# Performance work log

Hardware: AMD Instinct MI355X
Metric: run time of the kernel (lower is better)

The kernel has to match this reference:

```python
import jax, jax.numpy as jnp
import numpy as np

B, N, IN_DIM, EMB, HEADS, M, ITERS = 8, 4096, 1024, 512, 4, 256, 6
DH = EMB // HEADS
SCALE = DH ** -0.5
RES_K = 33  # residual depthwise conv kernel size (TransMIL / nystrom-attention default)


def setup_inputs() -> dict:
    key = jax.random.key(0)
    ks = iter(jax.random.split(key, 40))
    def rn(shape, s=0.02):
        return jax.random.normal(next(ks), shape, jnp.float32) * s
    inp = {"X": jax.random.normal(next(ks), (B, N, IN_DIM), jnp.float32)}
    inp["few_w"] = rn((IN_DIM, EMB)); inp["few_b"] = jnp.zeros((EMB,), jnp.float32)
    inp["cls_token"] = rn((1, 1, EMB), 1.0)
    for i in (1, 2):
        inp[f"l{i}_ln_g"] = jnp.ones((EMB,), jnp.float32)
        inp[f"l{i}_ln_b"] = jnp.zeros((EMB,), jnp.float32)
        inp[f"l{i}_qkv_w"] = rn((EMB, 3 * EMB))
        inp[f"l{i}_out_w"] = rn((EMB, EMB))
        inp[f"l{i}_out_b"] = jnp.zeros((EMB,), jnp.float32)
        inp[f"l{i}_res_k"] = rn((HEADS, 1, RES_K, 1))
    for ksz in (7, 5, 3):
        inp[f"ppeg_k{ksz}"] = rn((EMB, 1, ksz, ksz))
        inp[f"ppeg_b{ksz}"] = jnp.zeros((EMB,), jnp.float32)
    inp["norm_g"] = jnp.ones((EMB,), jnp.float32)
    inp["norm_b"] = jnp.zeros((EMB,), jnp.float32)
    inp["cls_w"] = rn((EMB, 1)); inp["cls_b"] = jnp.zeros((1,), jnp.float32)
    return inp


def _ln(x, g, b):
    mu = x.mean(-1, keepdims=True)
    var = x.var(-1, keepdims=True)
    return (x - mu) / jnp.sqrt(var + 1e-5) * g + b


def _pinv(x, iters):
    # Moore-Penrose iterative pseudo-inverse of (..., m, m)
    abs_x = jnp.abs(x)
    z = jnp.swapaxes(x, -1, -2) / (abs_x.sum(-1).max() * abs_x.sum(-2).max())
    I = jnp.eye(x.shape[-1], dtype=x.dtype)
    for _ in range(iters):
        xz = x @ z
        z = 0.25 * z @ (13 * I - xz @ (15 * I - xz @ (7 * I - xz)))
    return z


def _nystrom_layer(x, ln_g, ln_b, qkv_w, out_w, out_b, res_k):
    # pre-norm transformer layer with Nystrom attention + residual depthwise conv
    b, n, d = x.shape
    h = _ln(x, ln_g, ln_b)
    pad = (-n) % M  # left-pad so seq divisible by n_landmarks
    hp = jnp.pad(h, ((0, 0), (pad, 0), (0, 0)))
    n_p = n + pad
    q, k, v = jnp.split(hp @ qkv_w, 3, axis=-1)
    def to_heads(t):
        return t.reshape(b, n_p, HEADS, DH).transpose(0, 2, 1, 3)  # (b,h,n,dh)
    q, k, v = to_heads(q) * SCALE, to_heads(k), to_heads(v)
    l = n_p // M
    q_l = q.reshape(b, HEADS, M, l, DH).mean(3)  # landmark means
    k_l = k.reshape(b, HEADS, M, l, DH).mean(3)
    a1 = jax.nn.softmax(jnp.einsum('bhid,bhjd->bhij', q, k_l), -1)    # (b,h,n,m)
    a2 = jax.nn.softmax(jnp.einsum('bhid,bhjd->bhij', q_l, k_l), -1)  # (b,h,m,m)
    a3 = jax.nn.softmax(jnp.einsum('bhid,bhjd->bhij', q_l, k), -1)    # (b,h,m,n)
    out = a1 @ (_pinv(a2, ITERS) @ (a3 @ v))
    # residual depthwise conv over sequence, one channel per head
    res = jax.lax.conv_general_dilated(
        v, res_k, (1, 1), ((RES_K // 2, RES_K // 2), (0, 0)),
        dimension_numbers=('NCHW', 'OIHW', 'NCHW'), feature_group_count=HEADS)
    out = out + res
    out = out.transpose(0, 2, 1, 3).reshape(b, n_p, d) @ out_w + out_b
    return x + out[:, -n:]


def _dwconv(x, k, bias, pad):
    y = jax.lax.conv_general_dilated(
        x, k, (1, 1), ((pad, pad), (pad, pad)),
        dimension_numbers=('NCHW', 'OIHW', 'NCHW'), feature_group_count=EMB)
    return y + bias[None, :, None, None]


def _ppeg(x, H, W, k7, b7, k5, b5, k3, b3):
    b, _, c = x.shape
    cls_t, feat = x[:, :1], x[:, 1:]
    f = feat.transpose(0, 2, 1).reshape(b, c, H, W)
    y = f + _dwconv(f, k7, b7, 3) + _dwconv(f, k5, b5, 2) + _dwconv(f, k3, b3, 1)
    y = y.reshape(b, c, H * W).transpose(0, 2, 1)
    return jnp.concatenate([cls_t, y], axis=1)


def _forward(X, few_w, few_b, cls_token,
             l1_ln_g, l1_ln_b, l1_qkv_w, l1_out_w, l1_out_b, l1_res_k,
             l2_ln_g, l2_ln_b, l2_qkv_w, l2_out_w, l2_out_b, l2_res_k,
             ppeg_k7, ppeg_b7, ppeg_k5, ppeg_b5, ppeg_k3, ppeg_b3,
             norm_g, norm_b, cls_w, cls_b):
    b, bag = X.shape[0], X.shape[1]
    h = X @ few_w + few_b
    ps = int(np.ceil(np.sqrt(bag)))
    add = ps * ps - bag
    h = jnp.concatenate([h, h[:, :add]], axis=1)  # pad bag to perfect square
    h = jnp.concatenate([jnp.broadcast_to(cls_token, (b, 1, EMB)), h], axis=1)
    h = _nystrom_layer(h, l1_ln_g, l1_ln_b, l1_qkv_w, l1_out_w, l1_out_b, l1_res_k)
    h = _ppeg(h, ps, ps, ppeg_k7, ppeg_b7, ppeg_k5, ppeg_b5, ppeg_k3, ppeg_b3)
    h = _nystrom_layer(h, l2_ln_g, l2_ln_b, l2_qkv_w, l2_out_w, l2_out_b, l2_res_k)
    h = _ln(h, norm_g, norm_b)
    return (h[:, 0] @ cls_w + cls_b).squeeze(-1)  # (batch,) bag logits


def reference(X, few_w, few_b, cls_token,
              l1_ln_g, l1_ln_b, l1_qkv_w, l1_out_w, l1_out_b, l1_res_k,
              l2_ln_g, l2_ln_b, l2_qkv_w, l2_out_w, l2_out_b, l2_res_k,
              ppeg_k7, ppeg_b7, ppeg_k5, ppeg_b5, ppeg_k3, ppeg_b3,
              norm_g, norm_b, cls_w, cls_b):
    return _forward(X, few_w, few_b, cls_token,
                    l1_ln_g, l1_ln_b, l1_qkv_w, l1_out_w, l1_out_b, l1_res_k,
                    l2_ln_g, l2_ln_b, l2_qkv_w, l2_out_w, l2_out_b, l2_res_k,
                    ppeg_k7, ppeg_b7, ppeg_k5, ppeg_b5, ppeg_k3, ppeg_b3,
                    norm_g, norm_b, cls_w, cls_b)
```

## Files before the change

kernel.cpp:

```cpp
#include <hip/hip_runtime.h>

constexpr int BATCH = 8;
constexpr int NTOK  = 4097;
constexpr int NP    = 4352;
constexpr int PADR  = 255;
constexpr int EMBD  = 512;
constexpr int DHD   = 128;
constexpr int LSUB  = 17;
constexpr float SCALE_F = 0.08838834764831845f;

constexpr int PPS   = 72;
constexpr int PPLN  = 72 * 70;
constexpr long long TPAD_FLOATS = (long long)BATCH * EMBD * PPLN;

typedef unsigned short u16;
typedef short   s16x8 __attribute__((ext_vector_type(8)));
typedef u16     u16x4 __attribute__((ext_vector_type(4)));
typedef float   f32x4 __attribute__((ext_vector_type(4)));

__device__ __forceinline__ u16 f2bf(float x) {
    unsigned u = __float_as_uint(x);
    u += 0x7fffu + ((u >> 16) & 1u);
    return (u16)(u >> 16);
}
__device__ __forceinline__ float bf2f(u16 h) {
    return __uint_as_float(((unsigned)h) << 16);
}

__device__ __forceinline__ void gload16(const u16* gp, u16* lp) {
    __builtin_amdgcn_global_load_lds(
        (const __attribute__((address_space(1))) unsigned int*)gp,
        (__attribute__((address_space(3))) unsigned int*)lp,
        16, 0, 0);
}

__device__ __forceinline__ float block_sum256(float v) {
    __shared__ float tmp[4];
    __syncthreads();
#pragma unroll
    for (int off = 32; off > 0; off >>= 1) v += __shfl_down(v, off, 64);
    int t = threadIdx.x;
    if ((t & 63) == 0) tmp[t >> 6] = v;
    __syncthreads();
    return tmp[0] + tmp[1] + tmp[2] + tmp[3];
}

__device__ __forceinline__ float block_max256(float v) {
    __shared__ float tmp[4];
    __syncthreads();
#pragma unroll
    for (int off = 32; off > 0; off >>= 1) v = fmaxf(v, __shfl_down(v, off, 64));
    int t = threadIdx.x;
    if ((t & 63) == 0) tmp[t >> 6] = v;
    __syncthreads();
    return fmaxf(fmaxf(tmp[0], tmp[1]), fmaxf(tmp[2], tmp[3]));
}

struct GemmP {
    const float* A; const float* B; float* C; const float* bias;
    long long As1, As2, Bs1, Bs2, Cs1, Cs2;
    int Adiv, Bdiv, Cdiv;
    int Am, Bk, Bn, Cm, Arow, Crow;
    int M, N, K, nb;
    float alpha; int accum;
    float bdiagc; int btrans; float cdiagc; int ctrans;
};

constexpr int LDSTR = 40;
constexpr int AH = 0, AL = 2560, BHs = 5120, BLs = 7680;

__global__ __launch_bounds__(256) void gemm_k(GemmP p) {
    __shared__ u16 lds[10240];
    const int bz = blockIdx.z;
    const float* Ab = p.A + (long long)(bz / p.Adiv) * p.As1 + (long long)(bz % p.Adiv) * p.As2;
    const float* Bb = p.B + (long long)(bz / p.Bdiv) * p.Bs1 + (long long)(bz % p.Bdiv) * p.Bs2;
    float*       Cb = p.C + (long long)(bz / p.Cdiv) * p.Cs1 + (long long)(bz % p.Cdiv) * p.Cs2;
    const int m0 = blockIdx.y * 64, n0 = blockIdx.x * 64;
    const int t = threadIdx.x;
    const int wave = t >> 6, lane = t & 63;
    const int wm = (wave & 1) * 32, wn = (wave >> 1) * 32;
    const int quad = lane >> 4, l15 = lane & 15;

    f32x4 acc[2][2];
#pragma unroll
    for (int i = 0; i < 2; ++i)
#pragma unroll
        for (int j = 0; j < 2; ++j) acc[i][j] = (f32x4){0.f, 0.f, 0.f, 0.f};

    for (int k0 = 0; k0 < p.K; k0 += 32) {
        {
            const int ar = t >> 2, ac = (t & 3) * 8;
            float v[8];
            if (m0 + ar < p.M) {
                const float* s = Ab + (long long)(m0 + ar + p.Arow) * p.Am + (k0 + ac);
                float4 x0 = *(const float4*)s, x1 = *(const float4*)(s + 4);
                v[0] = x0.x; v[1] = x0.y; v[2] = x0.z; v[3] = x0.w;
                v[4] = x1.x; v[5] = x1.y; v[6] = x1.z; v[7] = x1.w;
            } else {
#pragma unroll
                for (int i = 0; i < 8; ++i) v[i] = 0.f;
            }
            u16 h[8], l[8];
#pragma unroll
            for (int i = 0; i < 8; ++i) { h[i] = f2bf(v[i]); l[i] = f2bf(v[i] - bf2f(h[i])); }
            const int off = ar * LDSTR + ac;
            u16x4 a0, a1, b0, b1;
#pragma unroll
            for (int i = 0; i < 4; ++i) { a0[i] = h[i]; a1[i] = h[i + 4]; b0[i] = l[i]; b1[i] = l[i + 4]; }
            *(u16x4*)&lds[AH + off] = a0; *(u16x4*)&lds[AH + off + 4] = a1;
            *(u16x4*)&lds[AL + off] = b0; *(u16x4*)&lds[AL + off + 4] = b1;
        }
        if (p.Bn == 1) {
            const int bk = t >> 3, n8 = (t & 7) * 8;
            const float* s = Bb + (long long)(k0 + bk) * p.Bk + (n0 + n8);
            float4 x0 = *(const float4*)s, x1 = *(const float4*)(s + 4);
            float v[8] = {x0.x, x0.y, x0.z, x0.w, x1.x, x1.y, x1.z, x1.w};
            if (p.btrans) {
                const int gk = k0 + bk;
#pragma unroll
                for (int i = 0; i < 8; ++i)
                    v[i] = (gk == n0 + n8 + i ? p.bdiagc : 0.f) - v[i];
            }
#pragma unroll
            for (int i = 0; i < 8; ++i) {
                int j = (i + (t & 7)) & 7;
                u16 h = f2bf(v[j]);
                lds[BHs + (n8 + j) * LDSTR + bk] = h;
                lds[BLs + (n8 + j) * LDSTR + bk] = f2bf(v[j] - bf2f(h));
            }
        } else {
            const int bn = t >> 2, k8 = (t & 3) * 8;
            const float* s = Bb + (long long)(n0 + bn) * p.Bn + (k0 + k8);
            float4 x0 = *(const float4*)s, x1 = *(const float4*)(s + 4);
            float v[8] = {x0.x, x0.y, x0.z, x0.w, x1.x, x1.y, x1.z, x1.w};
            u16 h[8], l[8];
#pragma unroll
            for (int i = 0; i < 8; ++i) { h[i] = f2bf(v[i]); l[i] = f2bf(v[i] - bf2f(h[i])); }
            const int off = bn * LDSTR + k8;
            u16x4 a0, a1, b0, b1;
#pragma unroll
            for (int i = 0; i < 4; ++i) { a0[i] = h[i]; a1[i] = h[i + 4]; b0[i] = l[i]; b1[i] = l[i + 4]; }
            *(u16x4*)&lds[BHs + off] = a0; *(u16x4*)&lds[BHs + off + 4] = a1;
            *(u16x4*)&lds[BLs + off] = b0; *(u16x4*)&lds[BLs + off + 4] = b1;
        }
        __syncthreads();

        s16x8 ah[2], al[2], bh[2], bl[2];
#pragma unroll
        for (int mi = 0; mi < 2; ++mi) {
            const int off = (wm + mi * 16 + l15) * LDSTR + quad * 8;
            u16x4 q0 = *(const u16x4*)&lds[AH + off], q1 = *(const u16x4*)&lds[AH + off + 4];
            u16x4 r0 = *(const u16x4*)&lds[AL + off], r1 = *(const u16x4*)&lds[AL + off + 4];
            s16x8 fh, fl;
#pragma unroll
            for (int i = 0; i < 4; ++i) { fh[i] = q0[i]; fh[i + 4] = q1[i]; fl[i] = r0[i]; fl[i + 4] = r1[i]; }
            ah[mi] = fh; al[mi] = fl;
        }
#pragma unroll
        for (int ni = 0; ni < 2; ++ni) {
            const int off = (wn + ni * 16 + l15) * LDSTR + quad * 8;
            u16x4 q0 = *(const u16x4*)&lds[BHs + off], q1 = *(const u16x4*)&lds[BHs + off + 4];
            u16x4 r0 = *(const u16x4*)&lds[BLs + off], r1 = *(const u16x4*)&lds[BLs + off + 4];
            s16x8 fh, fl;
#pragma unroll
            for (int i = 0; i < 4; ++i) { fh[i] = q0[i]; fh[i + 4] = q1[i]; fl[i] = r0[i]; fl[i + 4] = r1[i]; }
            bh[ni] = fh; bl[ni] = fl;
        }
#pragma unroll
        for (int mi = 0; mi < 2; ++mi)
#pragma unroll
            for (int ni = 0; ni < 2; ++ni) {
                acc[mi][ni] = __builtin_amdgcn_mfma_f32_16x16x32_bf16(ah[mi], bh[ni], acc[mi][ni], 0, 0, 0);
                acc[mi][ni] = __builtin_amdgcn_mfma_f32_16x16x32_bf16(ah[mi], bl[ni], acc[mi][ni], 0, 0, 0);
                acc[mi][ni] = __builtin_amdgcn_mfma_f32_16x16x32_bf16(al[mi], bh[ni], acc[mi][ni], 0, 0, 0);
            }
        __syncthreads();
    }

#pragma unroll
    for (int mi = 0; mi < 2; ++mi)
#pragma unroll
        for (int ni = 0; ni < 2; ++ni) {
            const int n = n0 + wn + ni * 16 + l15;
#pragma unroll
            for (int r = 0; r < 4; ++r) {
                const int m = m0 + wm + mi * 16 + quad * 4 + r;
                if (m >= p.M) continue;
                float v = p.alpha * acc[mi][ni][r];
                if (p.bias) v += p.bias[n];
                if (p.ctrans) v = (m == n ? p.cdiagc : 0.f) - v;
                float* dst = Cb + (long long)(m + p.Crow) * p.Cm + n;
                if (p.accum) *dst += v; else *dst = v;
            }
        }
}

struct SplitP {
    const float* src; u16* dh; u16* dl;
    long long s1, s2, rstride, dstride, total;
    int div, R, C8;
    float scale;
};
__global__ __launch_bounds__(256) void split_k(SplitP p) {
    long long idx = (long long)blockIdx.x * 256 + threadIdx.x;
    if (idx >= p.total) return;
    int c8 = (int)(idx % p.C8);
    long long tmp = idx / p.C8;
    int r  = (int)(tmp % p.R);
    int bz = (int)(tmp / p.R);
    const float* s = p.src + (long long)(bz / p.div) * p.s1 + (long long)(bz % p.div) * p.s2
                   + (long long)r * p.rstride + c8 * 8;
    float4 x0 = *(const float4*)s, x1 = *(const float4*)(s + 4);
    float v[8] = {x0.x, x0.y, x0.z, x0.w, x1.x, x1.y, x1.z, x1.w};
    s16x8 hv, lv;
#pragma unroll
    for (int i = 0; i < 8; ++i) {
        float sv = v[i] * p.scale;
        u16 h = f2bf(sv);
        hv[i] = (short)h;
        lv[i] = (short)f2bf(sv - bf2f(h));
    }
    long long doff = (long long)bz * p.dstride + (long long)r * (p.C8 * 8) + c8 * 8;
    *(s16x8*)&p.dh[doff] = hv;
    *(s16x8*)&p.dl[doff] = lv;
}

__global__ __launch_bounds__(256) void splitT_k(const float* __restrict__ src,
                                                u16* __restrict__ dh, u16* __restrict__ dl,
                                                int K, int N) {
    int idx = blockIdx.x * 256 + threadIdx.x;
    if (idx >= N * K) return;
    int n = idx / K, k = idx - n * K;
    float v = src[(long long)k * N + n];
    u16 h = f2bf(v);
    dh[idx] = h;
    dl[idx] = f2bf(v - bf2f(h));
}

struct GemmBtP {
    const u16 *Ah, *Al, *Bh, *Bl;
    float* C; const float* bias;
    long long Abs, Bbs, Cbs;
    int M, N, K, Cm, Crow, accum;
};

__global__ __launch_bounds__(512, 4) void gemm_bt_k(GemmBtP p) {
    __shared__ __align__(16) u16 lds[32768];
    const int bz = blockIdx.z;
    const u16* Ahb = p.Ah + (long long)bz * p.Abs;
    const u16* Alb = p.Al + (long long)bz * p.Abs;
    const u16* Bhb = p.Bh + (long long)bz * p.Bbs;
    const u16* Blb = p.Bl + (long long)bz * p.Bbs;
    float*     Cb  = p.C  + (long long)bz * p.Cbs;

    const int NX = gridDim.x;
    const int nwg = NX * gridDim.y;
    const int bid = blockIdx.y * NX + blockIdx.x;
    const int qq = nwg >> 3, rr = nwg & 7;
    const int xcd = bid & 7, loc = bid >> 3;
    const int nbid = (xcd < rr) ? (xcd * (qq + 1) + loc)
                                : (rr * (qq + 1) + (xcd - rr) * qq + loc);
    const int m0 = (nbid / NX) * 128, n0 = (nbid % NX) * 256;

    const int t = threadIdx.x;
    const int wave = t >> 6, lane = t & 63;
    const int wm = (wave & 1) * 64, wn = (wave >> 1) * 64;
    const int quad = lane >> 4, l15 = lane & 15;
    const int K = p.K;

    const int lrow = lane >> 3;
    const int jx   = (lane & 7) ^ lrow;
    const int r0   = wave * 16 + lrow;
    const int sga0 = (m0 + r0     < p.M) ? (m0 + r0)     : (p.M - 1);
    const int sga1 = (m0 + r0 + 8 < p.M) ? (m0 + r0 + 8) : (p.M - 1);
    const long long sb0 = (long long)sga0 * K + jx * 8;
    const long long sb1 = (long long)sga1 * K + jx * 8;
    u16* ldsw = &lds[wave * 1024];

    const long long bb0   = (long long)(n0 + wn + l15) * K + quad * 8;
    const long long bstep = 16LL * K;

    f32x4 acc[4][4];
#pragma unroll
    for (int i = 0; i < 4; ++i)
#pragma unroll
        for (int j = 0; j < 4; ++j) acc[i][j] = (f32x4){0.f, 0.f, 0.f, 0.f};

    auto STAGE = [&](int buf, int ko) {
        u16* d = ldsw + buf * 16384;
        gload16(Ahb + sb0 + ko, d);
        gload16(Ahb + sb1 + ko, d + 512);
        gload16(Alb + sb0 + ko, d + 8192);
        gload16(Alb + sb1 + ko, d + 8192 + 512);
    };

    STAGE(0, 0);
    __syncthreads();

    const int nt = K >> 6;
    int cur = 0;
    for (int t0 = 0; t0 < nt; ++t0) {
        const int k0 = t0 << 6;
        if (t0 + 1 < nt) STAGE(cur ^ 1, k0 + 64);
        const int bufo = cur * 16384;
#pragma unroll
        for (int kh = 0; kh < 2; ++kh) {
            s16x8 bh[4], bl[4];
#pragma unroll
            for (int ni = 0; ni < 4; ++ni) {
                const long long bo = bb0 + ni * bstep + k0 + kh * 32;
                bh[ni] = *(const s16x8*)&Bhb[bo];
                bl[ni] = *(const s16x8*)&Blb[bo];
            }
#pragma unroll
            for (int mi = 0; mi < 4; ++mi) {
                const int r  = wm + mi * 16 + l15;
                const int c8 = kh * 4 + quad;
                const int off = bufo + r * 64 + ((c8 ^ (r & 7)) << 3);
                s16x8 ah = *(const s16x8*)&lds[off];
                s16x8 al = *(const s16x8*)&lds[off + 8192];
#pragma unroll
                for (int ni = 0; ni < 4; ++ni) {
                    acc[mi][ni] = __builtin_amdgcn_mfma_f32_16x16x32_bf16(ah, bh[ni], acc[mi][ni], 0, 0, 0);
                    acc[mi][ni] = __builtin_amdgcn_mfma_f32_16x16x32_bf16(ah, bl[ni], acc[mi][ni], 0, 0, 0);
                    acc[mi][ni] = __builtin_amdgcn_mfma_f32_16x16x32_bf16(al, bh[ni], acc[mi][ni], 0, 0, 0);
                }
            }
        }
        __syncthreads();
        cur ^= 1;
    }

#pragma unroll
    for (int mi = 0; mi < 4; ++mi)
#pragma unroll
        for (int ni = 0; ni < 4; ++ni) {
            const int n = n0 + wn + ni * 16 + l15;
            const float bv = p.bias ? p.bias[n] : 0.f;
#pragma unroll
            for (int r = 0; r < 4; ++r) {
                const int m = m0 + wm + mi * 16 + quad * 4 + r;
                if (m >= p.M) continue;
                float* dst = Cb + (long long)(m + p.Crow) * p.Cm + n;
                float v = acc[mi][ni][r] + bv;
                if (p.accum) *dst += v; else *dst = v;
            }
        }
}

__global__ void cls_set_k(float* H0, const float* cls) {
    int t = blockIdx.x * 256 + threadIdx.x;
    int b = t >> 9, c = t & 511;
    H0[(long long)b * NTOK * EMBD + c] = cls[c];
}

__global__ __launch_bounds__(256) void ln_pad_k(const float* __restrict__ H0,
                                                u16* __restrict__ oh, u16* __restrict__ ol,
                                                const float* g, const float* bb) {
    int row = blockIdx.x, b = blockIdx.y, t = threadIdx.x;
    long long off = ((long long)b * NP + row) * EMBD;
    if (row < PADR) {
        oh[off + t] = 0; oh[off + t + 256] = 0;
        ol[off + t] = 0; ol[off + t + 256] = 0;
        return;
    }
    const float* x = H0 + ((long long)b * NTOK + (row - PADR)) * EMBD;
    float v0 = x[t], v1 = x[t + 256];
    float mu = block_sum256(v0 + v1) * (1.f / EMBD);
    float d0 = v0 - mu, d1 = v1 - mu;
    float var = block_sum256(d0 * d0 + d1 * d1) * (1.f / EMBD);
    float rs = 1.f / sqrtf(var + 1e-5f);
    float y0 = d0 * rs * g[t]       + bb[t];
    float y1 = d1 * rs * g[t + 256] + bb[t + 256];
    u16 h0 = f2bf(y0); oh[off + t]       = h0; ol[off + t]       = f2bf(y0 - bf2f(h0));
    u16 h1 = f2bf(y1); oh[off + t + 256] = h1; ol[off + t + 256] = f2bf(y1 - bf2f(h1));
}

__global__ void landmark_k(const float* __restrict__ QKV, float* __restrict__ QL,
                           float* __restrict__ KL) {
    long long idx = (long long)blockIdx.x * 256 + threadIdx.x;
    int d = idx & 127; int i = (int)((idx >> 7) & 255); int bh = (int)(idx >> 15);
    int b = bh >> 2, h = bh & 3;
    const float* base = QKV + (long long)b * NP * 1536 + (long long)i * LSUB * 1536 + h * DHD + d;
    float sq = 0.f, sk = 0.f;
#pragma unroll
    for (int j = 0; j < LSUB; ++j) { sq += base[j * 1536]; sk += base[j * 1536 + EMBD]; }
    QL[idx] = sq * (1.f / LSUB);
    KL[idx] = sk * (1.f / LSUB);
}

__global__ __launch_bounds__(256) void softmax256_k(float* __restrict__ X) {
    long long row = (long long)blockIdx.x * 4 + (threadIdx.x >> 6);
    int lane = threadIdx.x & 63;
    float4* p = (float4*)(X + row * 256) + lane;
    float4 v = *p;
    float m = fmaxf(fmaxf(v.x, v.y), fmaxf(v.z, v.w));
#pragma unroll
    for (int off = 32; off > 0; off >>= 1) m = fmaxf(m, __shfl_xor(m, off, 64));
    float ex = __expf(v.x - m), ey = __expf(v.y - m), ez = __expf(v.z - m), ew = __expf(v.w - m);
    float s = ex + ey + ez + ew;
#pragma unroll
    for (int off = 32; off > 0; off >>= 1) s += __shfl_xor(s, off, 64);
    float inv = 1.f / s;
    *p = make_float4(ex * inv, ey * inv, ez * inv, ew * inv);
}

__global__ __launch_bounds__(256) void softmax_lds_k(float* __restrict__ X) {
    __shared__ float rowbuf[4352];
    float4* p  = (float4*)(X + (long long)blockIdx.x * 4352);
    float4* r4 = (float4*)rowbuf;
    const int t = threadIdx.x;
    float m = -1e30f;
    for (int i = t; i < 1088; i += 256) {
        float4 v = p[i]; r4[i] = v;
        m = fmaxf(m, fmaxf(fmaxf(v.x, v.y), fmaxf(v.z, v.w)));
    }
    m = block_max256(m);
    float s = 0.f;
    for (int i = t; i < 1088; i += 256) {
        float4 v = r4[i];
        v.x = __expf(v.x - m); v.y = __expf(v.y - m); v.z = __expf(v.z - m); v.w = __expf(v.w - m);
        r4[i] = v;
        s += v.x + v.y + v.z + v.w;
    }
    s = block_sum256(s);
    float inv = 1.f / s;
    for (int i = t; i < 1088; i += 256) {
        float4 v = r4[i];
        p[i] = make_float4(v.x * inv, v.y * inv, v.z * inv, v.w * inv);
    }
}

__global__ __launch_bounds__(256) void pinv_absmax_k(const float* __restrict__ X, float* red) {
    int bh = blockIdx.x, t = threadIdx.x;
    const float* x = X + (long long)bh * 65536;
    float rs = 0.f, cs = 0.f;
    for (int j = 0; j < 256; ++j) { rs += fabsf(x[t * 256 + j]); cs += fabsf(x[j * 256 + t]); }
    float mr = block_max256(rs);
    float mc = block_max256(cs);
    if (t == 0) { red[bh] = mr; red[32 + bh] = mc; }
}

__global__ void pinv_scalar_k(const float* red, float* inv) {
    float mr = 0.f, mc = 0.f;
    for (int i = 0; i < 32; ++i) { mr = fmaxf(mr, red[i]); mc = fmaxf(mc, red[32 + i]); }
    inv[0] = 1.f / (mr * mc);
}

__global__ void pinv_tinit_k(const float* __restrict__ X, const float* __restrict__ inv,
                             float* __restrict__ Z) {
    long long idx = (long long)blockIdx.x * 256 + threadIdx.x;
    int j = (int)(idx & 255); int i = (int)((idx >> 8) & 255); long long bh = idx >> 16;
    Z[idx] = X[(bh << 16) + ((long long)j << 8) + i] * inv[0];
}

__global__ void resconv_k(const float* __restrict__ QKV, const float* __restrict__ rk,
                          float* __restrict__ ATT2) {
    long long idx = (long long)blockIdx.x * 256 + threadIdx.x;
    if (idx >= (long long)BATCH * NTOK * EMBD) return;
    int c = (int)(idx & 511); long long r = idx >> 9;
    int n = PADR + (int)(r % NTOK); int b = (int)(r / NTOK);
    int h = c >> 7, d = c & 127;
    const float* vb = QKV + (long long)b * NP * 1536 + 1024 + h * DHD + d;
    float acc = 0.f;
#pragma unroll
    for (int u = 0; u < 33; ++u) {
        int nn = n + u - 16;
        if (nn >= 0 && nn < NP) acc += vb[(long long)nn * 1536] * rk[h * 33 + u];
    }
    ATT2[((long long)b * NP + n) * EMBD + c] += acc;
}

__global__ void wsum_k(const float* __restrict__ k7, const float* __restrict__ k5,
                       const float* __restrict__ k3, const float* __restrict__ b7,
                       const float* __restrict__ b5, const float* __restrict__ b3,
                       float* __restrict__ W) {
    int idx = blockIdx.x * 256 + threadIdx.x;
    if (idx < 25088) {
        int c = idx / 49, i = idx - c * 49;
        int dy = i / 7, dx = i - dy * 7;
        float w = k7[idx];
        if (dy >= 1 && dy <= 5 && dx >= 1 && dx <= 5) w += k5[c * 25 + (dy - 1) * 5 + (dx - 1)];
        if (dy >= 2 && dy <= 4 && dx >= 2 && dx <= 4) w += k3[c * 9 + (dy - 2) * 3 + (dx - 2)];
        W[idx] = w;
    } else if (idx < 25600) {
        int c = idx - 25088;
        W[25088 + c] = b7[c] + b5[c] + b3[c];
    }
}

__global__ __launch_bounds__(256) void tin_k(const float* __restrict__ H0,
                                             float* __restrict__ Tpad) {
    __shared__ float lds[64][65];
    const int y = blockIdx.x, c0 = blockIdx.y * 64, b = blockIdx.z;
    const int t = threadIdx.x;
    const int pc = t & 63, pr4 = t >> 6;
    const float* src = H0 + ((long long)b * NTOK + 1 + y * 64) * EMBD + c0;
#pragma unroll
    for (int i = 0; i < 16; ++i) {
        int pr = pr4 + i * 4;
        lds[pr][pc] = src[(long long)pr * EMBD + pc];
    }
    __syncthreads();
    const int xw = t & 63, cw4 = t >> 6;
#pragma unroll
    for (int i = 0; i < 16; ++i) {
        int cw = cw4 + i * 4;
        Tpad[(long long)(b * 512 + c0 + cw) * PPLN + (3 + y) * PPS + 3 + xw] = lds[xw][cw];
    }
}

__global__ __launch_bounds__(256, 4) void conv7_k(const float* __restrict__ Tpad,
                                                  const float* __restrict__ Wall,
                                                  float* __restrict__ Tout) {
    const int bc = blockIdx.x;
    const int c = bc & 511;
    const int t = threadIdx.x;
    const int x = t & 63, band = t >> 6;
    const int y0 = band * 16;
    const float* in = Tpad + (long long)bc * PPLN + x;
    float* outp = Tout + (long long)bc * 4096 + x;

    float W[49];
#pragma unroll
    for (int i = 0; i < 49; ++i) W[i] = Wall[c * 49 + i];
    const float bias = Wall[25088 + c];

    float win[7][7];
#pragma unroll
    for (int j = 0; j < 6; ++j)
#pragma unroll
        for (int d = 0; d < 7; ++d)
            win[j][d] = in[(y0 + j) * PPS + d];

#pragma unroll
    for (int yy = 0; yy < 16; ++yy) {
        const int slot = (6 + yy) % 7;
#pragma unroll
        for (int d = 0; d < 7; ++d)
            win[slot][d] = in[(y0 + yy + 6) * PPS + d];
        float s = bias + win[(yy + 3) % 7][3];
#pragma unroll
        for (int dy = 0; dy < 7; ++dy) {
            const int r = (yy + dy) % 7;
#pragma unroll
            for (int dx = 0; dx < 7; ++dx)
                s += W[dy * 7 + dx] * win[r][dx];
        }
        outp[(y0 + yy) * 64] = s;
    }
}

__global__ __launch_bounds__(256) void tout_k(const float* __restrict__ Tout,
                                              float* __restrict__ H0) {
    __shared__ float lds[64][65];
    const int y = blockIdx.x, c0 = blockIdx.y * 64, b = blockIdx.z;
    const int t = threadIdx.x;
    const int xl = t & 63, cl4 = t >> 6;
#pragma unroll
    for (int i = 0; i < 16; ++i) {
        int cl = cl4 + i * 4;
        lds[xl][cl] = Tout[(long long)(b * 512 + c0 + cl) * 4096 + y * 64 + xl];
    }
    __syncthreads();
    const int pc = t & 63, pl4 = t >> 6;
    float* dst = H0 + ((long long)b * NTOK + 1 + y * 64) * EMBD + c0;
#pragma unroll
    for (int i = 0; i < 16; ++i) {
        int pl = pl4 + i * 4;
        dst[(long long)pl * EMBD + pc] = lds[pl][pc];
    }
}

__global__ __launch_bounds__(256) void head_k(const float* __restrict__ H0, const float* g,
                                              const float* bb, const float* cw, const float* cb,
                                              float* __restrict__ out) {
    int b = blockIdx.x, t = threadIdx.x;
    const float* x = H0 + (long long)b * NTOK * EMBD;
    float v0 = x[t], v1 = x[t + 256];
    float mu = block_sum256(v0 + v1) * (1.f / EMBD);
    float d0 = v0 - mu, d1 = v1 - mu;
    float var = block_sum256(d0 * d0 + d1 * d1) * (1.f / EMBD);
    float rs = 1.f / sqrtf(var + 1e-5f);
    float y0 = d0 * rs * g[t] + bb[t];
    float y1 = d1 * rs * g[t + 256] + bb[t + 256];
    float s = block_sum256(y0 * cw[t] + y1 * cw[t + 256]);
    if (t == 0) out[b] = s + cb[0];
}

extern "C" void kernel_launch(void* const* d_in, const int* in_sizes, int n_in,
                              void* d_out, int out_size, void* d_ws, size_t ws_size,
                              hipStream_t stream) {
    (void)in_sizes; (void)n_in; (void)out_size; (void)ws_size;
    const float* X        = (const float*)d_in[0];
    const float* few_w    = (const float*)d_in[1];
    const float* few_b    = (const float*)d_in[2];
    const float* cls_tok  = (const float*)d_in[3];
    const float* ln_g[2]  = {(const float*)d_in[4],  (const float*)d_in[10]};
    const float* ln_b[2]  = {(const float*)d_in[5],  (const float*)d_in[11]};
    const float* qkv_w[2] = {(const float*)d_in[6],  (const float*)d_in[12]};
    const float* out_w[2] = {(const float*)d_in[7],  (const float*)d_in[13]};
    const float* out_b[2] = {(const float*)d_in[8],  (const float*)d_in[14]};
    const float* res_k[2] = {(const float*)d_in[9],  (const float*)d_in[15]};
    const float* k7 = (const float*)d_in[16]; const float* b7 = (const float*)d_in[17];
    const float* k5 = (const float*)d_in[18]; const float* b5 = (const float*)d_in[19];
    const float* k3 = (const float*)d_in[20]; const float* b3 = (const float*)d_in[21];
    const float* norm_g = (const float*)d_in[22]; const float* norm_b = (const float*)d_in[23];
    const float* cls_w  = (const float*)d_in[24]; const float* cls_b  = (const float*)d_in[25];
    float* out = (float*)d_out;

    float* ws  = (float*)d_ws;
    float* H0  = ws;
    float* LNH = H0  + 16781312LL;
    float* QKV = LNH + 17825792LL;
    float* A3  = QKV + 53477376LL;
    float* QL  = A3  + 35651584LL;
    float* KL  = QL  + 1048576LL;
    float* A2  = KL  + 1048576LL;
    float* KV  = A2  + 2097152LL;
    float* ZKV = KV  + 1048576LL;
    float* RED = ZKV + 1048576LL;

    u16* LNHh = (u16*)LNH;
    u16* LNHl = (u16*)(LNH + 8912896LL);
    u16* QLh  = (u16*)KV;
    u16* QLl  = (u16*)(KV + 524288LL);
    u16* KLh  = (u16*)ZKV;
    u16* KLl  = (u16*)(ZKV + 524288LL);
    u16* Xh   = (u16*)A3;
    u16* Xl   = (u16*)(A3 + 16777216LL);
    u16* ATh  = (u16*)A3;
    u16* ATl  = (u16*)(A3 + 8390656LL);
    u16* Wh   = (u16*)A2;
    u16* fwl  = (u16*)(A2 + 262144LL);
    u16* qwl  = (u16*)(A2 + 393216LL);
    u16* owl  = (u16*)(A2 + 131072LL);
    float* Zb0 = LNH;
    float* Zb1 = LNH + 2097152LL;
    float* XZm = LNH + 4194304LL;
    float* U1  = LNH + 6291456LL;
    float* U2  = LNH + 8388608LL;
    float* Tpad = QKV;
    float* Tout = QKV + TPAD_FLOATS;
    float* WSUM = A3;

    auto gemmx = [&](const float* A, long long As1, long long As2, int Adiv, int Am, int Arow,
                     const float* Bm, long long Bs1, long long Bs2, int Bdiv, int Bk, int Bn,
                     float* C, long long Cs1, long long Cs2, int Cdiv, int Cm, int Crow,
                     int M, int N, int K, int nb, float alpha, int accum, const float* bias,
                     float bdiagc, int btrans, float cdiagc, int ctrans) {
        GemmP p;
        p.A = A; p.B = Bm; p.C = C; p.bias = bias;
        p.As1 = As1; p.As2 = As2; p.Bs1 = Bs1; p.Bs2 = Bs2; p.Cs1 = Cs1; p.Cs2 = Cs2;
        p.Adiv = Adiv; p.Bdiv = Bdiv; p.Cdiv = Cdiv;
        p.Am = Am; p.Bk = Bk; p.Bn = Bn; p.Cm = Cm; p.Arow = Arow; p.Crow = Crow;
        p.M = M; p.N = N; p.K = K; p.nb = nb; p.alpha = alpha; p.accum = accum;
        p.bdiagc = bdiagc; p.btrans = btrans; p.cdiagc = cdiagc; p.ctrans = ctrans;
        dim3 grid(N / 64, (M + 63) / 64, nb);
        gemm_k<<<grid, 256, 0, stream>>>(p);
    };
    auto gemm = [&](const float* A, long long As1, long long As2, int Adiv, int Am, int Arow,
                    const float* Bm, long long Bs1, long long Bs2, int Bdiv, int Bk, int Bn,
                    float* C, long long Cs1, long long Cs2, int Cdiv, int Cm, int Crow,
                    int M, int N, int K, int nb, float alpha, int accum, const float* bias) {
        gemmx(A, As1, As2, Adiv, Am, Arow, Bm, Bs1, Bs2, Bdiv, Bk, Bn,
              C, Cs1, Cs2, Cdiv, Cm, Crow, M, N, K, nb, alpha, accum, bias, 0.f, 0, 0.f, 0);
    };
    auto split = [&](const float* src, u16* dh, u16* dl, long long s1, long long s2, int div,
                     long long rstride, int R, int C, int nb, float scale) {
        SplitP p;
        p.src = src; p.dh = dh; p.dl = dl;
        p.s1 = s1; p.s2 = s2; p.div = div;
        p.rstride = rstride; p.R = R; p.C8 = C >> 3;
        p.dstride = (long long)R * C;
        p.total = (long long)nb * R * (C >> 3);
        p.scale = scale;
        int blocks = (int)((p.total + 255) / 256);
        split_k<<<blocks, 256, 0, stream>>>(p);
    };
    auto gemmbt = [&](const u16* Ah, const u16* Al, long long Abs,
                      const u16* Bh, const u16* Bl, long long Bbs,
                      float* C, long long Cbs, int Cm, int Crow,
                      int M, int N, int K, int nb, int accum, const float* bias) {
        GemmBtP p;
        p.Ah = Ah; p.Al = Al; p.Bh = Bh; p.Bl = Bl;
        p.C = C; p.bias = bias;
        p.Abs = Abs; p.Bbs = Bbs; p.Cbs = Cbs;
        p.M = M; p.N = N; p.K = K; p.Cm = Cm; p.Crow = Crow; p.accum = accum;
        dim3 grid(N / 256, (M + 127) / 128, nb);
        gemm_bt_k<<<grid, 512, 0, stream>>>(p);
    };

    cls_set_k<<<16, 256, 0, stream>>>(H0, cls_tok);
    split(X, Xh, Xl, 0, 0, 1, 1024, 32768, 1024, 1, 1.f);
    splitT_k<<<2048, 256, 0, stream>>>(few_w, Wh, fwl, 1024, 512);
    gemmbt(Xh, Xl, 4194304LL, Wh, fwl, 0,
           H0, 2097664LL, 512, 1,
           4096, 512, 1024, BATCH, 0, few_b);

    for (int L = 0; L < 2; ++L) {
        ln_pad_k<<<dim3(NP, BATCH), 256, 0, stream>>>(H0, LNHh, LNHl, ln_g[L], ln_b[L]);
        splitT_k<<<3072, 256, 0, stream>>>(qkv_w[L], Wh, qwl, 512, 1536);
        gemmbt(LNHh, LNHl, 0, Wh, qwl, 0,
               QKV, 0, 1536, 0,
               34816, 1536, 512, 1, 0, nullptr);
        landmark_k<<<4096, 256, 0, stream>>>(QKV, QL, KL);
        gemm(QL, 32768LL, 0, 1, 128, 0,
             KL, 32768LL, 0, 1, 1, 128,
             A2, 65536LL, 0, 1, 256, 0,
             256, 256, 128, 32, SCALE_F, 0, nullptr);
        softmax256_k<<<2048, 256, 0, stream>>>(A2);
        split(QL, QLh, QLl, 32768LL, 0, 1, 128, 256, 128, 32, SCALE_F);
        split(KL, KLh, KLl, 32768LL, 0, 1, 128, 256, 128, 32, 1.f);
        split(QKV + 512, LNHh, LNHl, 6680064LL, 128LL, 4, 1536, 4352, 128, 32, 1.f);
        gemmbt(QLh, QLl, 32768LL, LNHh, LNHl, 557056LL,
               A3, 1114112LL, 4352, 0,
               256, 4352, 128, 32, 0, nullptr);
        softmax_lds_k<<<8192, 256, 0, stream>>>(A3);
        gemm(A3, 1114112LL, 0, 1, 4352, 0,
             QKV + 1024, 6680064LL, 128LL, 4, 1536, 1,
             KV, 32768LL, 0, 1, 128, 0,
             256, 128, 4352, 32, 1.f, 0, nullptr);
        split(QKV, LNHh, LNHl, 6680064LL, 128LL, 4, 1536, 4352, 128, 32, SCALE_F);
        gemmbt(LNHh, LNHl, 557056LL, KLh, KLl, 32768LL,
               A3, 1114112LL, 256, 0,
               4352, 256, 128, 32, 0, nullptr);
        softmax256_k<<<34816, 256, 0, stream>>>(A3);
        pinv_absmax_k<<<32, 256, 0, stream>>>(A2, RED);
        pinv_scalar_k<<<1, 1, 0, stream>>>(RED, RED + 64);
        pinv_tinit_k<<<8192, 256, 0, stream>>>(A2, RED + 64, Zb0);
        float* zc = Zb0; float* zn = Zb1;
        for (int it = 0; it < 6; ++it) {
            gemm(A2, 65536LL, 0, 1, 256, 0, zc, 65536LL, 0, 1, 256, 1,
                 XZm, 65536LL, 0, 1, 256, 0, 256, 256, 256, 32, 1.f, 0, nullptr);
            gemmx(XZm, 65536LL, 0, 1, 256, 0, XZm, 65536LL, 0, 1, 256, 1,
                  U1, 65536LL, 0, 1, 256, 0, 256, 256, 256, 32, 1.f, 0, nullptr,
                  7.f, 1, 15.f, 1);
            gemmx(XZm, 65536LL, 0, 1, 256, 0, U1, 65536LL, 0, 1, 256, 1,
                  U2, 65536LL, 0, 1, 256, 0, 256, 256, 256, 32, 1.f, 0, nullptr,
                  0.f, 0, 13.f, 1);
            gemm(zc, 65536LL, 0, 1, 256, 0, U2, 65536LL, 0, 1, 256, 1,
                 zn, 65536LL, 0, 1, 256, 0, 256, 256, 256, 32, 0.25f, 0, nullptr);
            float* t2 = zc; zc = zn; zn = t2;
        }
        gemm(zc, 65536LL, 0, 1, 256, 0,
             KV, 32768LL, 0, 1, 128, 1,
             ZKV, 32768LL, 0, 1, 128, 0,
             256, 128, 256, 32, 1.f, 0, nullptr);
        gemm(A3, 1114112LL, 0, 1, 256, 0,
             ZKV, 32768LL, 0, 1, 128, 1,
             LNH, 2228224LL, 128LL, 4, 512, 0,
             4352, 128, 256, 32, 1.f, 0, nullptr);
        resconv_k<<<65552, 256, 0, stream>>>(QKV, res_k[L], LNH);
        split(LNH + PADR * 512, ATh, ATl, 2228224LL, 0, 1, 512, 4097, 512, 8, 1.f);
        splitT_k<<<1024, 256, 0, stream>>>(out_w[L], Wh, owl, 512, 512);
        gemmbt(ATh, ATl, 2097664LL, Wh, owl, 0,
               H0, 2097664LL, 512, 0,
               4097, 512, 512, BATCH, 1, out_b[L]);

        if (L == 0) {
            hipMemsetAsync(Tpad, 0, TPAD_FLOATS * sizeof(float), stream);
            wsum_k<<<101, 256, 0, stream>>>(k7, k5, k3, b7, b5, b3, WSUM);
            tin_k<<<dim3(64, 8, 8), 256, 0, stream>>>(H0, Tpad);
            conv7_k<<<4096, 256, 0, stream>>>(Tpad, WSUM, Tout);
            tout_k<<<dim3(64, 8, 8), 256, 0, stream>>>(Tout, H0);
        }
    }

    head_k<<<BATCH, 256, 0, stream>>>(H0, norm_g, norm_b, cls_w, cls_b, out);
}
```

Measured before the change: 4.493 ms.

## Restructure bf16x3 GEMM to K=32 stages with register double-buffered B prefetch

The GEMM kernel's A staging shrinks from 64-wide K tiles to 32-wide tiles, which halves LDS use and removes the XOR swizzle. B fragments are now double-buffered in registers and prefetched one stage ahead, overlapping global B loads with MFMA work. The launch-bounds occupancy hint is dropped. Keeping two B buffers raises register pressure, and the shorter stages mean two barriers per 64 K elements. The unswizzled LDS layout may also cause bank conflicts.

```diff
diff --git a/kernel.cpp b/kernel.cpp
--- a/kernel.cpp
+++ b/kernel.cpp
@@ -244,8 +244,8 @@
     int M, N, K, Cm, Crow, accum;
 };
 
-__global__ __launch_bounds__(512, 4) void gemm_bt_k(GemmBtP p) {
-    __shared__ __align__(16) u16 lds[32768];
+__global__ __launch_bounds__(512) void gemm_bt_k(GemmBtP p) {
+    __shared__ __align__(16) u16 lds[16384];
     const int bz = blockIdx.z;
     const u16* Ahb = p.Ah + (long long)bz * p.Abs;
     const u16* Alb = p.Al + (long long)bz * p.Abs;
@@ -268,14 +268,10 @@
     const int quad = lane >> 4, l15 = lane & 15;
     const int K = p.K;
 
-    const int lrow = lane >> 3;
-    const int jx   = (lane & 7) ^ lrow;
-    const int r0   = wave * 16 + lrow;
-    const int sga0 = (m0 + r0     < p.M) ? (m0 + r0)     : (p.M - 1);
-    const int sga1 = (m0 + r0 + 8 < p.M) ? (m0 + r0 + 8) : (p.M - 1);
-    const long long sb0 = (long long)sga0 * K + jx * 8;
-    const long long sb1 = (long long)sga1 * K + jx * 8;
-    u16* ldsw = &lds[wave * 1024];
+    const int srow = 16 * wave + (lane >> 2);
+    const int sga  = (m0 + srow < p.M) ? (m0 + srow) : (p.M - 1);
+    const long long sbase = (long long)sga * K + (lane & 3) * 8;
+    u16* ldsw = &lds[wave * 512];
 
     const long long bb0   = (long long)(n0 + wn + l15) * K + quad * 8;
     const long long bstep = 16LL * K;
@@ -286,49 +282,51 @@
 #pragma unroll
         for (int j = 0; j < 4; ++j) acc[i][j] = (f32x4){0.f, 0.f, 0.f, 0.f};
 
+    s16x8 bh0[4], bl0[4], bh1[4], bl1[4];
+
     auto STAGE = [&](int buf, int ko) {
-        u16* d = ldsw + buf * 16384;
-        gload16(Ahb + sb0 + ko, d);
-        gload16(Ahb + sb1 + ko, d + 512);
-        gload16(Alb + sb0 + ko, d + 8192);
-        gload16(Alb + sb1 + ko, d + 8192 + 512);
+        u16* d = ldsw + buf * 8192;
+        gload16(Ahb + sbase + ko, d);
+        gload16(Alb + sbase + ko, d + 4096);
     };
+    auto LOADB = [&](int ko, s16x8 (&bh)[4], s16x8 (&bl)[4]) {
+#pragma unroll
+        for (int ni = 0; ni < 4; ++ni) {
+            const long long bo = bb0 + ni * bstep + ko;
+            bh[ni] = *(const s16x8*)&Bhb[bo];
+            bl[ni] = *(const s16x8*)&Blb[bo];
+        }
+    };
+    auto COMPUTE = [&](int bufo, s16x8 (&bh)[4], s16x8 (&bl)[4]) {
+#pragma unroll
+        for (int mi = 0; mi < 4; ++mi) {
+            const int off = bufo + (wm + mi * 16 + l15) * 32 + quad * 8;
+            s16x8 ah = *(const s16x8*)&lds[off];
+            s16x8 al = *(const s16x8*)&lds[off + 4096];
+#pragma unroll
+            for (int ni = 0; ni < 4; ++ni) {
+                acc[mi][ni] = __builtin_amdgcn_mfma_f32_16x16x32_bf16(ah, bh[ni], acc[mi][ni], 0, 0, 0);
+                acc[mi][ni] = __builtin_amdgcn_mfma_f32_16x16x32_bf16(ah, bl[ni], acc[mi][ni], 0, 0, 0);
+                acc[mi][ni] = __builtin_amdgcn_mfma_f32_16x16x32_bf16(al, bh[ni], acc[mi][ni], 0, 0, 0);
+            }
+        }
+    };
 
     STAGE(0, 0);
+    LOADB(0, bh0, bl0);
     __syncthreads();
 
-    const int nt = K >> 6;
-    int cur = 0;
-    for (int t0 = 0; t0 < nt; ++t0) {
-        const int k0 = t0 << 6;
-        if (t0 + 1 < nt) STAGE(cur ^ 1, k0 + 64);
-        const int bufo = cur * 16384;
-#pragma unroll
-        for (int kh = 0; kh < 2; ++kh) {
-            s16x8 bh[4], bl[4];
-#pragma unroll
-            for (int ni = 0; ni < 4; ++ni) {
-                const long long bo = bb0 + ni * bstep + k0 + kh * 32;
-                bh[ni] = *(const s16x8*)&Bhb[bo];
-                bl[ni] = *(const s16x8*)&Blb[bo];
-            }
-#pragma unroll
-            for (int mi = 0; mi < 4; ++mi) {
-                const int r  = wm + mi * 16 + l15;
-                const int c8 = kh * 4 + quad;
-                const int off = bufo + r * 64 + ((c8 ^ (r & 7)) << 3);
-                s16x8 ah = *(const s16x8*)&lds[off];
-                s16x8 al = *(const s16x8*)&lds[off + 8192];
-#pragma unroll
-                for (int ni = 0; ni < 4; ++ni) {
-                    acc[mi][ni] = __builtin_amdgcn_mfma_f32_16x16x32_bf16(ah, bh[ni], acc[mi][ni], 0, 0, 0);
-                    acc[mi][ni] = __builtin_amdgcn_mfma_f32_16x16x32_bf16(ah, bl[ni], acc[mi][ni], 0, 0, 0);
-                    acc[mi][ni] = __builtin_amdgcn_mfma_f32_16x16x32_bf16(al, bh[ni], acc[mi][ni], 0, 0, 0);
-                }
-            }
-        }
+    for (int k0 = 0; k0 < K; k0 += 64) {
+        STAGE(1, k0 + 32);
+        LOADB(k0 + 32, bh1, bl1);
+        COMPUTE(0, bh0, bl0);
         __syncthreads();
-        cur ^= 1;
+        if (k0 + 64 < K) {
+            STAGE(0, k0 + 64);
+            LOADB(k0 + 64, bh0, bl0);
+        }
+        COMPUTE(8192, bh1, bl1);
+        __syncthreads();
     }
 
 #pragma unroll
```

New measurement: 4.636 ms. 3.2% more time.
